# Optimization experiments

Measured on AMD Instinct MI355X. Metric: run time of the kernel, lower is better.

The kernel has to match this reference:

```python
import jax, jax.numpy as jnp
import numpy as np

NUM_KNOTS = 10
DEGREE = 3
NUM_BASIS = NUM_KNOTS + DEGREE - 1  # 12
IN_FEATURES = 512
OUT_FEATURES = 512


def _interval_bounds():
    # t = linspace(0,1,num_knots); segment i covers [t[max(0,i-deg+1)], t[min(i+1,K-1)])
    t = np.linspace(0.0, 1.0, NUM_KNOTS, dtype=np.float32)
    idx = np.arange(NUM_BASIS)
    lower = t[np.maximum(0, idx - (DEGREE - 1))]
    upper = t[np.minimum(idx + 1, NUM_KNOTS - 1)]
    return jnp.asarray(lower), jnp.asarray(upper)


def setup_inputs() -> dict:
    key = jax.random.key(0)
    kx, kc = jax.random.split(key)
    x = jax.random.uniform(kx, (8, 2048, IN_FEATURES), dtype=jnp.float32)
    # coeffs for spline (i=out, j=in): torch indexes splines[i*in_features+j]
    coeffs = jax.random.normal(kc, (OUT_FEATURES, IN_FEATURES, NUM_BASIS), dtype=jnp.float32)
    return {"x": x, "coeffs": coeffs}


def reference(x, coeffs):
    lower, upper = _interval_bounds()  # [NUM_BASIS] each
    # piecewise-constant basis masks: [b, s, in, NUM_BASIS]
    xe = x[..., None]
    basis = ((xe >= lower) & (xe < upper)).astype(x.dtype)
    # out[b,s,i] = sum_j sum_k basis[b,s,j,k] * coeffs[i,j,k]
    return jnp.einsum("bsjk,ijk->bsi", basis, coeffs)
```

## Files before the change

kernel.cpp:

```cpp
#include <hip/hip_runtime.h>

#define MTOT 16384
#define NFEAT 512
#define KTOT 4608

typedef float f32x4 __attribute__((ext_vector_type(4)));
typedef short s16x8 __attribute__((ext_vector_type(8)));

__device__ __forceinline__ int div9(int c) { return (c * 7282) >> 16; }

#define GLDS(GP, LP) __builtin_amdgcn_global_load_lds( \
    (const __attribute__((address_space(1))) void*)(GP), \
    (__attribute__((address_space(3))) void*)(LP), 16, 0, 0)

__device__ __forceinline__ s16x8 decode_frag(unsigned code) {
  unsigned nb0 = code & 15u, nb1 = code >> 4;
  unsigned p0 = nb0 - 1u, p1 = nb1 - 1u;
  unsigned long long v0 = (nb0 ? 0x3F80ull : 0ull) << ((p0 & 3u) << 4);
  unsigned long long v1 = (nb1 ? 0x3F80ull : 0ull) << ((p1 & 3u) << 4);
  unsigned long long lo = (p0 < 4u ? v0 : 0ull) | (p1 < 4u ? v1 : 0ull);
  unsigned long long hi = (p0 < 4u ? 0ull : v0) | (p1 < 4u ? 0ull : v1);
  union { unsigned long long q[2]; s16x8 v; } u;
  u.q[0] = lo; u.q[1] = hi;
  return u.v;
}

__global__ __launch_bounds__(256) void prep(const float* __restrict__ x,
                                            const float* __restrict__ coeffs,
                                            unsigned char* __restrict__ codeT,
                                            unsigned short* __restrict__ Bmat) {
  __shared__ unsigned char segt[64][68];
  const int bx = blockIdx.x;
  const int tid = threadIdx.x;
  if (bx < 2048) {
    const int i = bx >> 2, q = bx & 3;
    const float* cb = coeffs + (size_t)i * 6144;
#pragma unroll
    for (int p = 0; p < 5; ++p) {
      int kl = p * 256 + tid;
      if (kl < 1152) {
        int k = q * 1152 + kl;
        int j = div9(k), s = k - j * 9;
        float v = cb[j * 12 + s] + cb[j * 12 + s + 1] + cb[j * 12 + s + 2];
        unsigned u = __float_as_uint(v);
        unsigned rn = (u + 0x7FFFu + ((u >> 16) & 1u)) >> 16;
        Bmat[(size_t)i * KTOT + k] = (unsigned short)rn;
      }
    }
  } else {
    const int bb = bx - 2048;
    const int mt = bb >> 3;
    const int jt = bb & 7;
    const int m0 = mt * 64;
    const float4* x4 = (const float4*)x;
    const float T1 = (float)(1.0/9.0), T2 = (float)(2.0/9.0), T3 = (float)(3.0/9.0),
                T4 = (float)(4.0/9.0), T5 = (float)(5.0/9.0), T6 = (float)(6.0/9.0),
                T7 = (float)(7.0/9.0), T8 = (float)(8.0/9.0);
#pragma unroll
    for (int it = 0; it < 4; ++it) {
      int f = it * 256 + tid;
      int m = f >> 4, jq = f & 15;
      float4 v = x4[(size_t)(m0 + m) * 128 + jt * 16 + jq];
      uchar4 sv;
      { float xv = v.x; sv.x = (unsigned char)((xv>=T1)+(xv>=T2)+(xv>=T3)+(xv>=T4)+(xv>=T5)+(xv>=T6)+(xv>=T7)+(xv>=T8)); }
      { float xv = v.y; sv.y = (unsigned char)((xv>=T1)+(xv>=T2)+(xv>=T3)+(xv>=T4)+(xv>=T5)+(xv>=T6)+(xv>=T7)+(xv>=T8)); }
      { float xv = v.z; sv.z = (unsigned char)((xv>=T1)+(xv>=T2)+(xv>=T3)+(xv>=T4)+(xv>=T5)+(xv>=T6)+(xv>=T7)+(xv>=T8)); }
      { float xv = v.w; sv.w = (unsigned char)((xv>=T1)+(xv>=T2)+(xv>=T3)+(xv>=T4)+(xv>=T5)+(xv>=T6)+(xv>=T7)+(xv>=T8)); }
      *(uchar4*)&segt[m][jq * 4] = sv;
    }
    __syncthreads();
#pragma unroll
    for (int p = 0; p < 5; ++p) {
      int u = p * 256 + tid;
      if (u < 1152) {
        int gl = u >> 4, mq = u & 15;
        int c0 = jt * 576 + gl * 8;
        int j0 = div9(c0), j1 = div9(c0 + 7);
        int j0l = j0 - jt * 64, j1l = j1 - jt * 64;
        uchar4 ob;
        unsigned char* pb = (unsigned char*)&ob;
#pragma unroll
        for (int c = 0; c < 4; ++c) {
          int m = mq + c * 16;
          int s0 = segt[m][j0l];
          int pos0 = j0 * 9 + s0 - c0;
          unsigned code = (pos0 >= 0 && pos0 < 8) ? (unsigned)(pos0 + 1) : 0u;
          if (j1 != j0) {
            int s1 = segt[m][j1l];
            int pos1 = j1 * 9 + s1 - c0;
            if (pos1 < 8) code |= (unsigned)(pos1 + 1) << 4;
          }
          pb[c] = (unsigned char)code;
        }
        *(uchar4*)(codeT + (size_t)(jt * 72 + gl) * MTOT + m0 + mq * 4) = ob;
      }
    }
  }
}

__global__ __launch_bounds__(256, 2) void kan_gemm(const unsigned char* __restrict__ codeT,
                                                   const unsigned short* __restrict__ Bmat,
                                                   float* __restrict__ out) {
  __shared__ __align__(16) short Blds[2][2][8192];
  __shared__ __align__(16) short lut[256 * 8];
  const int tid = threadIdx.x;
  const int lane = tid & 63;
  const int wid = tid >> 6;
  const int mh = wid & 1;
  const int kh = wid >> 1;
  const int lm = lane & 15;
  const int lq = lane >> 4;
  const int bx = blockIdx.x;
  const int mt = bx >> 2;
  const int nt = bx & 3;
  const int m0 = mt * 128, n0 = nt * 128;
  const int mb64 = m0 + mh * 64;

  { s16x8 v = decode_frag((unsigned)tid); *(s16x8*)&lut[tid * 8] = v; }

  const unsigned short* gBp = Bmat + (size_t)(n0 + mh * 64 + lm) * KTOT + kh * 2304 + lq * 8;
  const unsigned* gC0 = (const unsigned*)(codeT + (size_t)(kh * 288 + lq) * MTOT + mb64) + lm;
  const unsigned* gC1 = (const unsigned*)(codeT + (size_t)(kh * 288 + 4 + lq) * MTOT + mb64) + lm;

  f32x4 acc[4][8] = {};
  s16x8 af[8];
  unsigned crQ[2][2];

#define CRLOAD(SET) do { \
    crQ[SET][0] = gC0[0]; crQ[SET][1] = gC1[0]; \
    gC0 += 2 * MTOT; gC1 += 2 * MTOT; } while (0)

#define ISSUE_B(SLOT) do { \
    short* dst = &Blds[kh][SLOT][mh * 4096]; \
    GLDS(gBp,                 dst);        \
    GLDS(gBp + 32,            dst + 512);  \
    GLDS(gBp + 16 * KTOT,     dst + 1024); \
    GLDS(gBp + 16 * KTOT + 32, dst + 1536); \
    GLDS(gBp + 32 * KTOT,     dst + 2048); \
    GLDS(gBp + 32 * KTOT + 32, dst + 2560); \
    GLDS(gBp + 48 * KTOT,     dst + 3072); \
    GLDS(gBp + 48 * KTOT + 32, dst + 3584); \
    gBp += 64; } while (0)

#define DECODE(SET) do { \
    _Pragma("unroll") \
    for (int ms = 0; ms < 4; ++ms) { \
      af[ms * 2 + 0] = *(const s16x8*)&lut[((crQ[SET][0] >> (ms * 8)) & 255u) * 8]; \
      af[ms * 2 + 1] = *(const s16x8*)&lut[((crQ[SET][1] >> (ms * 8)) & 255u) * 8]; \
    } } while (0)

#define COMPUTE(SLOT) do { \
    __builtin_amdgcn_s_setprio(1); \
    _Pragma("unroll") \
    for (int ks = 0; ks < 2; ++ks) { \
      s16x8 bf[8]; \
      _Pragma("unroll") \
      for (int ns = 0; ns < 8; ++ns) \
        bf[ns] = *(const s16x8*)&Blds[kh][SLOT][(ns * 2 + ks) * 512 + lane * 8]; \
      _Pragma("unroll") \
      for (int ms = 0; ms < 4; ++ms) \
        _Pragma("unroll") \
        for (int ns = 0; ns < 8; ++ns) \
          acc[ms][ns] = __builtin_amdgcn_mfma_f32_16x16x32_bf16(af[ms * 2 + ks], bf[ns], acc[ms][ns], 0, 0, 0); \
    } \
    __builtin_amdgcn_s_setprio(0); } while (0)

  CRLOAD(0);
  ISSUE_B(0);
  __syncthreads();

#pragma unroll 1
  for (int tt = 0; tt < 18; ++tt) {
    ISSUE_B(1); CRLOAD(1);
    DECODE(0);
    COMPUTE(0);
    __syncthreads();
    if (tt < 17) { ISSUE_B(0); CRLOAD(0); }
    DECODE(1);
    COMPUTE(1);
    __syncthreads();
  }

  if (kh == 1) {
    float* p = (float*)(&Blds[0][0][0]) + mh * 8192;
#pragma unroll
    for (int ms = 0; ms < 4; ++ms)
#pragma unroll
      for (int ns = 0; ns < 8; ++ns)
#pragma unroll
        for (int rg = 0; rg < 4; ++rg)
          p[((ms * 8 + ns) * 4 + rg) * 64 + lane] = acc[ms][ns][rg];
  }
  __syncthreads();
  if (kh == 0) {
    const float* p = (const float*)(&Blds[0][0][0]) + mh * 8192;
#pragma unroll
    for (int ms = 0; ms < 4; ++ms)
#pragma unroll
      for (int ns = 0; ns < 8; ++ns) {
        int tok = mb64 + ms * 16 + lq * 4;
        int col = n0 + ns * 16 + lm;
        float* op = out + (size_t)tok * NFEAT + col;
#pragma unroll
        for (int rg = 0; rg < 4; ++rg)
          op[(size_t)rg * NFEAT] = acc[ms][ns][rg] + p[((ms * 8 + ns) * 4 + rg) * 64 + lane];
      }
  }
#undef CRLOAD
#undef ISSUE_B
#undef DECODE
#undef COMPUTE
}

extern "C" void kernel_launch(void* const* d_in, const int* in_sizes, int n_in,
                              void* d_out, int out_size, void* d_ws, size_t ws_size,
                              hipStream_t stream) {
  const float* x = (const float*)d_in[0];
  const float* coeffs = (const float*)d_in[1];
  float* out = (float*)d_out;
  unsigned char* codeT = (unsigned char*)d_ws;
  unsigned short* Bmat = (unsigned short*)((char*)d_ws + (size_t)576 * MTOT);

  prep<<<dim3(4096), dim3(256), 0, stream>>>(x, coeffs, codeT, Bmat);
  kan_gemm<<<dim3(512), dim3(256), 0, stream>>>(codeT, Bmat, out);
}
```

Measured before the change: 171.7 us.

## Software-pipeline LDS B-fragment reads and decode A fragments in registers

```diff
diff --git a/kernel.cpp b/kernel.cpp
--- a/kernel.cpp
+++ b/kernel.cpp
@@ -102,7 +102,6 @@
                                                    const unsigned short* __restrict__ Bmat,
                                                    float* __restrict__ out) {
   __shared__ __align__(16) short Blds[2][2][8192];
-  __shared__ __align__(16) short lut[256 * 8];
   const int tid = threadIdx.x;
   const int lane = tid & 63;
   const int wid = tid >> 6;
@@ -116,71 +115,93 @@
   const int m0 = mt * 128, n0 = nt * 128;
   const int mb64 = m0 + mh * 64;
 
-  { s16x8 v = decode_frag((unsigned)tid); *(s16x8*)&lut[tid * 8] = v; }
-
   const unsigned short* gBp = Bmat + (size_t)(n0 + mh * 64 + lm) * KTOT + kh * 2304 + lq * 8;
   const unsigned* gC0 = (const unsigned*)(codeT + (size_t)(kh * 288 + lq) * MTOT + mb64) + lm;
   const unsigned* gC1 = (const unsigned*)(codeT + (size_t)(kh * 288 + 4 + lq) * MTOT + mb64) + lm;
 
   f32x4 acc[4][8] = {};
-  s16x8 af[8];
-  unsigned crQ[2][2];
+  s16x8 bfP[8], bfQ[8];
+  unsigned crq[2][2];
 
 #define CRLOAD(SET) do { \
-    crQ[SET][0] = gC0[0]; crQ[SET][1] = gC1[0]; \
+    crq[SET][0] = gC0[0]; crq[SET][1] = gC1[0]; \
     gC0 += 2 * MTOT; gC1 += 2 * MTOT; } while (0)
 
 #define ISSUE_B(SLOT) do { \
     short* dst = &Blds[kh][SLOT][mh * 4096]; \
-    GLDS(gBp,                 dst);        \
-    GLDS(gBp + 32,            dst + 512);  \
-    GLDS(gBp + 16 * KTOT,     dst + 1024); \
+    GLDS(gBp,                  dst);        \
+    GLDS(gBp + 32,             dst + 512);  \
+    GLDS(gBp + 16 * KTOT,      dst + 1024); \
     GLDS(gBp + 16 * KTOT + 32, dst + 1536); \
-    GLDS(gBp + 32 * KTOT,     dst + 2048); \
+    GLDS(gBp + 32 * KTOT,      dst + 2048); \
     GLDS(gBp + 32 * KTOT + 32, dst + 2560); \
-    GLDS(gBp + 48 * KTOT,     dst + 3072); \
+    GLDS(gBp + 48 * KTOT,      dst + 3072); \
     GLDS(gBp + 48 * KTOT + 32, dst + 3584); \
     gBp += 64; } while (0)
 
-#define DECODE(SET) do { \
+#define RD(BF, SLOT, KSD) do { \
+    _Pragma("unroll") \
+    for (int ns = 0; ns < 8; ++ns) \
+      BF[ns] = *(const s16x8*)&Blds[kh][SLOT][(ns * 2 + (KSD)) * 512 + lane * 8]; \
+    } while (0)
+
+#define HALF(CRIDX, KSD, BF) do { \
+    __builtin_amdgcn_s_setprio(1); \
+    unsigned cw_ = crq[CRIDX][KSD]; \
     _Pragma("unroll") \
     for (int ms = 0; ms < 4; ++ms) { \
-      af[ms * 2 + 0] = *(const s16x8*)&lut[((crQ[SET][0] >> (ms * 8)) & 255u) * 8]; \
-      af[ms * 2 + 1] = *(const s16x8*)&lut[((crQ[SET][1] >> (ms * 8)) & 255u) * 8]; \
-    } } while (0)
-
-#define COMPUTE(SLOT) do { \
-    __builtin_amdgcn_s_setprio(1); \
-    _Pragma("unroll") \
-    for (int ks = 0; ks < 2; ++ks) { \
-      s16x8 bf[8]; \
+      s16x8 afv_ = decode_frag((cw_ >> (ms * 8)) & 255u); \
       _Pragma("unroll") \
       for (int ns = 0; ns < 8; ++ns) \
-        bf[ns] = *(const s16x8*)&Blds[kh][SLOT][(ns * 2 + ks) * 512 + lane * 8]; \
-      _Pragma("unroll") \
-      for (int ms = 0; ms < 4; ++ms) \
-        _Pragma("unroll") \
-        for (int ns = 0; ns < 8; ++ns) \
-          acc[ms][ns] = __builtin_amdgcn_mfma_f32_16x16x32_bf16(af[ms * 2 + ks], bf[ns], acc[ms][ns], 0, 0, 0); \
+        acc[ms][ns] = __builtin_amdgcn_mfma_f32_16x16x32_bf16(afv_, BF[ns], acc[ms][ns], 0, 0, 0); \
     } \
     __builtin_amdgcn_s_setprio(0); } while (0)
 
+#define VWAIT0() asm volatile("s_waitcnt vmcnt(0)" ::: "memory")
+#define BAR()    __builtin_amdgcn_s_barrier()
+
   CRLOAD(0);
   ISSUE_B(0);
-  __syncthreads();
+  VWAIT0();
+  BAR();
+  RD(bfP, 0, 0);
 
 #pragma unroll 1
-  for (int tt = 0; tt < 18; ++tt) {
-    ISSUE_B(1); CRLOAD(1);
-    DECODE(0);
-    COMPUTE(0);
-    __syncthreads();
-    if (tt < 17) { ISSUE_B(0); CRLOAD(0); }
-    DECODE(1);
-    COMPUTE(1);
-    __syncthreads();
-  }
-
+  for (int tt = 0; tt < 17; ++tt) {
+    BAR();
+    CRLOAD(1); ISSUE_B(1);
+    RD(bfQ, 0, 1);
+    HALF(0, 0, bfP);
+    VWAIT0();
+    BAR();
+    RD(bfP, 1, 0);
+    HALF(0, 1, bfQ);
+
+    BAR();
+    CRLOAD(0); ISSUE_B(0);
+    RD(bfQ, 1, 1);
+    HALF(1, 0, bfP);
+    VWAIT0();
+    BAR();
+    RD(bfP, 0, 0);
+    HALF(1, 1, bfQ);
+  }
+
+  BAR();
+  CRLOAD(1); ISSUE_B(1);
+  RD(bfQ, 0, 1);
+  HALF(0, 0, bfP);
+  VWAIT0();
+  BAR();
+  RD(bfP, 1, 0);
+  HALF(0, 1, bfQ);
+
+  BAR();
+  RD(bfQ, 1, 1);
+  HALF(1, 0, bfP);
+  HALF(1, 1, bfQ);
+
+  BAR();
   if (kh == 1) {
     float* p = (float*)(&Blds[0][0][0]) + mh * 8192;
 #pragma unroll
@@ -208,8 +229,10 @@
   }
 #undef CRLOAD
 #undef ISSUE_B
-#undef DECODE
-#undef COMPUTE
+#undef RD
+#undef HALF
+#undef VWAIT0
+#undef BAR
 }
 
 extern "C" void kernel_launch(void* const* d_in, const int* in_sizes, int n_in,
```

Measured after the change: 174.9 us. No clear change (+1.8%).
